# Kernel optimization log

Hardware: AMD Instinct MI355X
Metric: run time of the kernel (lower is better)

Reference implementation:

```python
import jax, jax.numpy as jnp
import numpy as np

N = 50000      # nodes
E = 800000     # edges (before self-loops)
G = 64         # graphs
F_IN = 128     # n_attr
OUT = 128      # size_vect
NEG_SLOPE = 0.2


def setup_inputs() -> dict:
    key = jax.random.key(0)
    ks = jax.random.split(key, 48)
    def rn(i, shape, s=0.05):
        return (jax.random.normal(ks[i], shape, jnp.float32) * s)
    x = jax.random.normal(ks[0], (N, F_IN), jnp.float32)
    src = jax.random.randint(ks[1], (E,), 0, N, jnp.int32)
    dst = jax.random.randint(ks[2], (E,), 0, N, jnp.int32)
    dst = jnp.where(dst == src, (dst + 1) % N, dst)  # no pre-existing self-loops
    edge_index = jnp.stack([src, dst])
    batch = jnp.sort(jax.random.randint(ks[3], (N,), 0, G, jnp.int32))
    inp = {"x": x, "edge_index": edge_index, "batch": batch}
    # GATConv params (heads=1): W [in,out], att_src/att_dst [out], bias [out]
    dims = [(F_IN, 64), (64, 128), (128, 256)]
    for li, (di, do) in enumerate(dims, start=1):
        b = 4 + (li - 1) * 4
        inp[f"W{li}"] = rn(b, (di, do))
        inp[f"asrc{li}"] = rn(b + 1, (do,))
        inp[f"adst{li}"] = rn(b + 2, (do,))
        inp[f"b{li}"] = rn(b + 3, (do,))
    # dense tail: Linear stored as [in,out]
    dense = {"d1": (512, 256), "d2": (256, 128), "d3": (128, 64),
             "mean": (256, 64), "d4": (64, 64), "d5": (64, 128),
             "d6": (128, 256), "d7": (256, OUT)}
    i = 20
    for name, (di, do) in dense.items():
        inp[f"{name}_w"] = rn(i, (di, do))
        inp[f"{name}_b"] = rn(i + 1, (do,))
        i += 2
    return inp


def _gat_conv(x, src, dst, W, a_src, a_dst, b):
    h = x @ W                                   # [N, out]
    e = (h @ a_src)[src] + (h @ a_dst)[dst]     # [E']
    e = jnp.where(e > 0, e, NEG_SLOPE * e)      # LeakyReLU(0.2)
    m = jax.ops.segment_max(e, dst, num_segments=N)
    ex = jnp.exp(e - m[dst])
    denom = jax.ops.segment_sum(ex, dst, num_segments=N)
    alpha = ex / denom[dst]                     # segment softmax over incoming edges
    out = jax.ops.segment_sum(h[src] * alpha[:, None], dst, num_segments=N)
    return out + b


def reference(x, edge_index, batch,
              W1, asrc1, adst1, b1, W2, asrc2, adst2, b2, W3, asrc3, adst3, b3,
              d1_w, d1_b, d2_w, d2_b, d3_w, d3_b, mean_w, mean_b,
              d4_w, d4_b, d5_w, d5_b, d6_w, d6_b, d7_w, d7_b):
    ar = jnp.arange(N, dtype=edge_index.dtype)
    src = jnp.concatenate([edge_index[0], ar])  # add self-loops (PyG default)
    dst = jnp.concatenate([edge_index[1], ar])
    h = _gat_conv(x, src, dst, W1, asrc1, adst1, b1)
    h = _gat_conv(h, src, dst, W2, asrc2, adst2, b2)
    h = _gat_conv(h, src, dst, W3, asrc3, adst3, b3)   # [N, 256]
    x1 = jax.ops.segment_max(h, batch, num_segments=G)
    x2 = jax.ops.segment_sum(h, batch, num_segments=G)
    cnt = jax.ops.segment_sum(jnp.ones((N,), h.dtype), batch, num_segments=G)
    x3 = x2 / jnp.maximum(cnt, 1.0)[:, None]
    z = jnp.concatenate([x1, x2], axis=-1)              # [G, 512]
    z = jax.nn.relu(z @ d1_w + d1_b)
    z = jax.nn.relu(z @ d2_w + d2_b)
    z = jax.nn.relu(z @ d3_w + d3_b)
    z = z * jax.nn.sigmoid(x3 @ mean_w + mean_b)
    z = jax.nn.relu(z @ d4_w + d4_b)                    # dropout = identity (eval)
    z = jax.nn.relu(z @ d5_w + d5_b)
    z = jax.nn.relu(z @ d6_w + d6_b)
    return z @ d7_w + d7_b
```

## Files before the change

kernel.cpp:

```cpp
#include <hip/hip_runtime.h>
#include <hip/hip_bf16.h>
#include <math.h>

#define NN 50000
#define NE 800000
#define NG 64
#define CAP 64

#define NBKT 49
#define BMAX 20480
#define EPB  3125
#define KE   13

typedef unsigned short u16;
typedef __attribute__((ext_vector_type(8))) short short8;
typedef __attribute__((ext_vector_type(4))) float f32x4;

__device__ __forceinline__ float bfu2f(u16 u) {
    return __uint_as_float((unsigned)u << 16);
}
__device__ __forceinline__ u16 f2bfu(float f) {
    __hip_bfloat16 h = __float2bfloat16(f);
    union { __hip_bfloat16 h; u16 u; } c; c.h = h; return c.u;
}

__device__ __forceinline__ unsigned fkey(float f) {
    unsigned u = __float_as_uint(f);
    return (u & 0x80000000u) ? ~u : (u | 0x80000000u);
}
__device__ __forceinline__ float fkey_inv(unsigned k) {
    return (k & 0x80000000u) ? __uint_as_float(k ^ 0x80000000u) : __uint_as_float(~k);
}

__global__ void k_init(int* __restrict__ deg, u16* __restrict__ srcsort, int IB,
                       const float* __restrict__ W0, const float* __restrict__ as0, const float* __restrict__ ad0,
                       u16* __restrict__ Wb0, float* __restrict__ wa0, float* __restrict__ wb0,
                       const float* __restrict__ W1, const float* __restrict__ as1, const float* __restrict__ ad1,
                       u16* __restrict__ Wb1, float* __restrict__ wa1, float* __restrict__ wb1,
                       const float* __restrict__ W2, const float* __restrict__ as2, const float* __restrict__ ad2,
                       const float* __restrict__ b2f, const float* __restrict__ b3f,
                       u16* __restrict__ Wcb, float* __restrict__ bcv,
                       float* __restrict__ wa2c, float* __restrict__ wb2c,
                       float* __restrict__ cst,
                       const int* __restrict__ src, const int* __restrict__ dst,
                       unsigned* __restrict__ ebuf, int* __restrict__ bcur) {
    __shared__ float pas[4], pbs[4];
    __shared__ int hist[NBKT], gbase[NBKT];
    int tid = threadIdx.x;
    if (blockIdx.x < IB) {
        int i = blockIdx.x * 256 + tid;
        if (i < NN) {
            deg[i] = 1;
            srcsort[i << 6] = (u16)i;
        }
        return;
    }
    int b = blockIdx.x - IB;
    if (b < 192) {
        const float *W, *asv, *adv; u16* Wb; float *wa, *wb; int k, dout;
        if (b < 128) { W = W0; asv = as0; adv = ad0; Wb = Wb0; wa = wa0; wb = wb0; k = b;       dout = 64;  }
        else         { W = W1; asv = as1; adv = ad1; Wb = Wb1; wa = wa1; wb = wb1; k = b - 128; dout = 128; }
        float pa = 0.f, pb = 0.f;
        for (int n = tid; n < dout; n += 256) {
            float w = W[(size_t)k * dout + n];
            Wb[(size_t)k * dout + n] = f2bfu(w);
            pa += w * asv[n];
            pb += w * adv[n];
        }
#pragma unroll
        for (int off = 32; off; off >>= 1) {
            pa += __shfl_xor(pa, off);
            pb += __shfl_xor(pb, off);
        }
        if ((tid & 63) == 0) { pas[tid >> 6] = pa; pbs[tid >> 6] = pb; }
        __syncthreads();
        if (tid == 0) {
            wa[k] = pas[0] + pas[1] + pas[2] + pas[3];
            wb[k] = pbs[0] + pbs[1] + pbs[2] + pbs[3];
        }
        return;
    }
    if (b < 256) {
        int k = b - 192;
        int o = tid;
        float wc = 0.f;
        const float* wrow = W1 + (size_t)k * 128;
#pragma unroll 4
        for (int j = 0; j < 128; j++) wc += wrow[j] * W2[(size_t)j * 256 + o];
        Wcb[(size_t)k * 256 + o] = f2bfu(wc);
        float pa = wc * as2[o];
        float pb = wc * ad2[o];
#pragma unroll
        for (int off = 32; off; off >>= 1) {
            pa += __shfl_xor(pa, off);
            pb += __shfl_xor(pb, off);
        }
        if ((tid & 63) == 0) { pas[tid >> 6] = pa; pbs[tid >> 6] = pb; }
        __syncthreads();
        if (tid == 0) {
            wa2c[k] = pas[0] + pas[1] + pas[2] + pas[3];
            wb2c[k] = pbs[0] + pbs[1] + pbs[2] + pbs[3];
        }
        return;
    }
    if (b == 256) {
        int o = tid;
        float t = 0.f;
#pragma unroll 4
        for (int j = 0; j < 128; j++) t += b2f[j] * W2[(size_t)j * 256 + o];
        bcv[o] = t + b3f[o];
        float ps = t * as2[o];
        float pt = t * ad2[o];
#pragma unroll
        for (int off = 32; off; off >>= 1) {
            ps += __shfl_xor(ps, off);
            pt += __shfl_xor(pt, off);
        }
        if ((tid & 63) == 0) { pas[tid >> 6] = ps; pbs[tid >> 6] = pt; }
        __syncthreads();
        if (tid == 0) {
            cst[0] = pas[0] + pas[1] + pas[2] + pas[3];
            cst[1] = pbs[0] + pbs[1] + pbs[2] + pbs[3];
        }
        return;
    }
    {
        int e0 = (b - 257) * EPB;
        if (tid < NBKT) hist[tid] = 0;
        __syncthreads();
        unsigned pk[KE];
        unsigned br[KE];
#pragma unroll
        for (int k = 0; k < KE; k++) {
            int e = tid + k * 256;
            pk[k] = 0; br[k] = 0xffffffffu;
            if (e < EPB) {
                int sv = src[e0 + e];
                int dv = dst[e0 + e];
                int bkt = dv >> 10;
                int r = atomicAdd(&hist[bkt], 1);
                pk[k] = (unsigned)sv | ((unsigned)(dv & 1023) << 16);
                br[k] = ((unsigned)bkt << 16) | (unsigned)r;
            }
        }
        __syncthreads();
        if (tid < NBKT) gbase[tid] = atomicAdd(&bcur[tid], hist[tid]);
        __syncthreads();
#pragma unroll
        for (int k = 0; k < KE; k++) {
            if (br[k] != 0xffffffffu) {
                int bkt = (int)(br[k] >> 16);
                int r   = (int)(br[k] & 0xffffu);
                ebuf[(size_t)bkt * BMAX + gbase[bkt] + r] = pk[k];
            }
        }
    }
}

template<int DIN, int DOUT, bool XF32, bool STIN>
__device__ __forceinline__ void gemm_body(int bx, const void* __restrict__ Xin,
                                          const u16* __restrict__ Wb,
                                          u16* __restrict__ Hb,
                                          const float* __restrict__ bias,
                                          const float* __restrict__ wav,
                                          const float* __restrict__ wbv,
                                          float* __restrict__ sout,
                                          float* __restrict__ tout) {
    constexpr int KS = DIN / 32;
    constexpr int CT = DOUT / 16;
    constexpr int TPW = CT / 4;
    constexpr int STRIDE = DIN + 16;
    __shared__ u16 Xs[64 * STRIDE];
    int tid = threadIdx.x, wave = tid >> 6, lane = tid & 63;
    int quad = lane >> 4, l15 = lane & 15;
    int n0 = bx * 64;

    short8 bfr[TPW][KS];
#pragma unroll
    for (int ct = 0; ct < TPW; ct++) {
        int nb = (wave * TPW + ct) * 16 + l15;
#pragma unroll
        for (int ks = 0; ks < KS; ks++) {
            int kb = ks * 32 + quad * 8;
            short8 b;
#pragma unroll
            for (int j = 0; j < 8; j++) b[j] = (short)Wb[(size_t)(kb + j) * DOUT + nb];
            bfr[ct][ks] = b;
        }
    }

    for (int c = tid; c < 64 * DIN / 8; c += 256) {
        int row = (c * 8) / DIN, col = (c * 8) % DIN;
        int rg = n0 + row; if (rg >= NN) rg = NN - 1;
        u16 v[8];
        if constexpr (XF32) {
            const float* p = (const float*)Xin + (size_t)rg * DIN + col;
            float4 f0 = *(const float4*)p;
            float4 f1 = *(const float4*)(p + 4);
            v[0] = f2bfu(f0.x); v[1] = f2bfu(f0.y); v[2] = f2bfu(f0.z); v[3] = f2bfu(f0.w);
            v[4] = f2bfu(f1.x); v[5] = f2bfu(f1.y); v[6] = f2bfu(f1.z); v[7] = f2bfu(f1.w);
            if constexpr (STIN) {
                float pa = f0.x * wav[col]     + f0.y * wav[col + 1]
                         + f0.z * wav[col + 2] + f0.w * wav[col + 3]
                         + f1.x * wav[col + 4] + f1.y * wav[col + 5]
                         + f1.z * wav[col + 6] + f1.w * wav[col + 7];
                float pb = f0.x * wbv[col]     + f0.y * wbv[col + 1]
                         + f0.z * wbv[col + 2] + f0.w * wbv[col + 3]
                         + f1.x * wbv[col + 4] + f1.y * wbv[col + 5]
                         + f1.z * wbv[col + 6] + f1.w * wbv[col + 7];
                constexpr int RT = DIN / 8;
#pragma unroll
                for (int off = RT / 2; off; off >>= 1) {
                    pa += __shfl_xor(pa, off);
                    pb += __shfl_xor(pb, off);
                }
                if ((tid & (RT - 1)) == 0 && (n0 + row) < NN) {
                    sout[n0 + row] = pa;
                    tout[n0 + row] = pb;
                }
            }
        } else {
            const u16* p = (const u16*)Xin + (size_t)rg * DIN + col;
            ushort4 a = *(const ushort4*)p;
            ushort4 b = *(const ushort4*)(p + 4);
            v[0] = a.x; v[1] = a.y; v[2] = a.z; v[3] = a.w;
            v[4] = b.x; v[5] = b.y; v[6] = b.z; v[7] = b.w;
        }
        u16* d = &Xs[row * STRIDE + col];
#pragma unroll
        for (int j = 0; j < 8; j++) d[j] = v[j];
    }
    __syncthreads();

#pragma unroll
    for (int rt = 0; rt < 4; rt++) {
        short8 afr[KS];
#pragma unroll
        for (int ks = 0; ks < KS; ks++)
            afr[ks] = *(const short8*)&Xs[(rt * 16 + l15) * STRIDE + ks * 32 + quad * 8];
#pragma unroll
        for (int ct = 0; ct < TPW; ct++) {
            f32x4 cf = {0.f, 0.f, 0.f, 0.f};
#pragma unroll
            for (int ks = 0; ks < KS; ks++)
                cf = __builtin_amdgcn_mfma_f32_16x16x32_bf16(afr[ks], bfr[ct][ks], cf, 0, 0, 0);
            int col = (wave * TPW + ct) * 16 + l15;
            float bv = bias ? bias[col] : 0.f;
            int rbase = n0 + rt * 16 + quad * 4;
#pragma unroll
            for (int reg = 0; reg < 4; reg++) {
                int r = rbase + reg;
                if (r < NN) Hb[(size_t)r * DOUT + col] = f2bfu(cf[reg] + bv);
            }
        }
    }
}

__global__ __launch_bounds__(256) void k_front(const unsigned* __restrict__ ebuf,
                                               const int* __restrict__ bcur,
                                               int* __restrict__ deg, u16* __restrict__ srcsort,
                                               const float* __restrict__ x_in,
                                               const u16* __restrict__ Wb0, u16* __restrict__ Hb,
                                               const float* __restrict__ wa, const float* __restrict__ wb,
                                               float* __restrict__ s, float* __restrict__ t) {
    int tid = threadIdx.x;
    if (blockIdx.x < NBKT) {
        __shared__ int cnt[1024];
        int bkt = blockIdx.x;
        int base = bkt << 10;
        for (int i = tid; i < 1024; i += 256) cnt[i] = 1;
        __syncthreads();
        int n = bcur[bkt];
        const unsigned* eb = ebuf + (size_t)bkt * BMAX;
        for (int e = tid; e < n; e += 256) {
            unsigned p = eb[e];
            int sv = (int)(p & 0xffffu);
            int dl = (int)(p >> 16);
            int pos = atomicAdd(&cnt[dl], 1);
            if (pos < CAP) srcsort[((base + dl) << 6) + pos] = (u16)sv;
        }
        __syncthreads();
        for (int i = tid; i < 1024; i += 256) {
            int node = base + i;
            if (node < NN) deg[node] = cnt[i];
        }
        return;
    }
    gemm_body<128, 64, true, true>(blockIdx.x - NBKT, x_in, Wb0, Hb, nullptr, wa, wb, s, t);
}

template<bool BIAS>
__global__ void k_agg1(const int* __restrict__ deg, const u16* __restrict__ srcsort,
                       const float* __restrict__ s, const float* __restrict__ t,
                       const u16* __restrict__ Hb, const float* __restrict__ bias,
                       u16* __restrict__ OUT, const float* __restrict__ wan,
                       const float* __restrict__ wbn, const float* __restrict__ cst,
                       float* __restrict__ sout, float* __restrict__ tout) {
    constexpr int GS = 8;
    constexpr int P  = 8;
    int node = blockIdx.x * 4 + (threadIdx.x >> 6);
    int lane = threadIdx.x & 63;
    if (node >= NN) return;
    int cnt = min(deg[node], CAP);
    float tn = t[node];
    int sv = 0; float ex = 0.f;
    if (lane < cnt) {
        sv = srcsort[(node << 6) + lane];
        float e = s[sv] + tn;
        e = (e > 0.f) ? e : 0.2f * e;
        ex = expf(e);
    }
    float dsum = ex;
#pragma unroll
    for (int off = 32; off; off >>= 1) dsum += __shfl_xor(dsum, off);
    ex *= 1.f / dsum;

    int sg = lane / GS;
    int pg = lane % GS;
    float acc[8];
#pragma unroll
    for (int e = 0; e < 8; e++) acc[e] = 0.f;

    for (int q = 0; q < cnt; q += P) {
        int myq = q + sg;
        int mq = (myq < cnt) ? myq : q;
        float a = __shfl(ex, mq);
        int  idx = __shfl(sv, mq);
        if (myq >= cnt) a = 0.f;
        uint4 u = *(const uint4*)(Hb + (size_t)idx * 64 + pg * 8);
        acc[0] += a * bfu2f((u16)(u.x & 0xffff));
        acc[1] += a * bfu2f((u16)(u.x >> 16));
        acc[2] += a * bfu2f((u16)(u.y & 0xffff));
        acc[3] += a * bfu2f((u16)(u.y >> 16));
        acc[4] += a * bfu2f((u16)(u.z & 0xffff));
        acc[5] += a * bfu2f((u16)(u.z >> 16));
        acc[6] += a * bfu2f((u16)(u.w & 0xffff));
        acc[7] += a * bfu2f((u16)(u.w >> 16));
    }

#pragma unroll
    for (int step = GS; step < 64; step <<= 1) {
#pragma unroll
        for (int e = 0; e < 8; e++) acc[e] += __shfl_xor(acc[e], step);
    }
    if constexpr (BIAS) {
#pragma unroll
        for (int e = 0; e < 8; e++) acc[e] += bias[pg * 8 + e];
    }

    {
        float pa = 0.f, pb = 0.f;
#pragma unroll
        for (int e = 0; e < 8; e++) {
            pa += acc[e] * wan[pg * 8 + e];
            pb += acc[e] * wbn[pg * 8 + e];
        }
#pragma unroll
        for (int off = 32; off; off >>= 1) {
            pa += __shfl_xor(pa, off);
            pb += __shfl_xor(pb, off);
        }
        if (lane == 0) {
            float cs = 0.f, ct_ = 0.f;
            if constexpr (!BIAS) { cs = cst[0]; ct_ = cst[1]; }
            sout[node] = pa * (1.f / P) + cs;
            tout[node] = pb * (1.f / P) + ct_;
        }
    }

    if (sg == 0) {
        uint4 o;
        o.x = (unsigned)f2bfu(acc[0]) | ((unsigned)f2bfu(acc[1]) << 16);
        o.y = (unsigned)f2bfu(acc[2]) | ((unsigned)f2bfu(acc[3]) << 16);
        o.z = (unsigned)f2bfu(acc[4]) | ((unsigned)f2bfu(acc[5]) << 16);
        o.w = (unsigned)f2bfu(acc[6]) | ((unsigned)f2bfu(acc[7]) << 16);
        *(uint4*)(OUT + (size_t)node * 64 + pg * 8) = o;
    }
}

__global__ __launch_bounds__(256) void k_aggemm_pool(const int* __restrict__ deg,
                                                     const u16* __restrict__ srcsort,
                                                     const float* __restrict__ s,
                                                     const float* __restrict__ t,
                                                     const u16* __restrict__ A2,
                                                     const u16* __restrict__ Wb,
                                                     const float* __restrict__ bias,
                                                     const int* __restrict__ batch,
                                                     unsigned* __restrict__ x1k,
                                                     float* __restrict__ x2,
                                                     float* __restrict__ cntg) {
    constexpr int DIN = 64, DOUT = 256;
    constexpr int KS = DIN / 32;
    constexpr int TPW = DOUT / 16 / 4;
    constexpr int STRIDE = DIN + 16;
    __shared__ u16 Xs[64 * STRIDE];
    __shared__ int gID[64];
    int tid = threadIdx.x, wave = tid >> 6, lane = tid & 63;
    int quad = lane >> 4, l15 = lane & 15;
    int n0 = blockIdx.x * 64;

    short8 bfr[TPW][KS];
#pragma unroll
    for (int ct = 0; ct < TPW; ct++) {
        int nb = (wave * TPW + ct) * 16 + l15;
#pragma unroll
        for (int ks = 0; ks < KS; ks++) {
            int kb = ks * 32 + quad * 8;
            short8 b;
#pragma unroll
            for (int j = 0; j < 8; j++) b[j] = (short)Wb[(size_t)(kb + j) * DOUT + nb];
            bfr[ct][ks] = b;
        }
    }

    if (tid < 64) {
        int rg = n0 + tid;
        gID[tid] = batch[(rg < NN) ? rg : (NN - 1)];
    }

    for (int i = 0; i < 16; i++) {
        int row = wave * 16 + i;
        int node = n0 + row;
        if (node < NN) {
            int cnt = min(deg[node], CAP);
            float tn = t[node];
            int sv = 0; float ex = 0.f;
            if (lane < cnt) {
                sv = srcsort[(node << 6) + lane];
                float e = s[sv] + tn;
                e = (e > 0.f) ? e : 0.2f * e;
                ex = expf(e);
            }
            float dsum = ex;
#pragma unroll
            for (int off = 32; off; off >>= 1) dsum += __shfl_xor(dsum, off);
            ex *= 1.f / dsum;

            int sg = lane / 8;
            int pg = lane % 8;
            float acc[8];
#pragma unroll
            for (int e = 0; e < 8; e++) acc[e] = 0.f;
            for (int q = 0; q < cnt; q += 8) {
                int myq = q + sg;
                int mq = (myq < cnt) ? myq : q;
                float a = __shfl(ex, mq);
                int  idx = __shfl(sv, mq);
                if (myq >= cnt) a = 0.f;
                uint4 u = *(const uint4*)(A2 + (size_t)idx * 64 + pg * 8);
                acc[0] += a * bfu2f((u16)(u.x & 0xffff));
                acc[1] += a * bfu2f((u16)(u.x >> 16));
                acc[2] += a * bfu2f((u16)(u.y & 0xffff));
                acc[3] += a * bfu2f((u16)(u.y >> 16));
                acc[4] += a * bfu2f((u16)(u.z & 0xffff));
                acc[5] += a * bfu2f((u16)(u.z >> 16));
                acc[6] += a * bfu2f((u16)(u.w & 0xffff));
                acc[7] += a * bfu2f((u16)(u.w >> 16));
            }
#pragma unroll
            for (int step = 8; step < 64; step <<= 1) {
#pragma unroll
                for (int e = 0; e < 8; e++) acc[e] += __shfl_xor(acc[e], step);
            }
            if (sg == 0) {
                u16* d = &Xs[row * STRIDE + pg * 8];
#pragma unroll
                for (int e = 0; e < 8; e++) d[e] = f2bfu(acc[e]);
            }
        } else {
            if (lane < 8) {
                u16* d = &Xs[row * STRIDE + lane * 8];
#pragma unroll
                for (int e = 0; e < 8; e++) d[e] = 0;
            }
        }
    }
    __syncthreads();

    f32x4 acc2[4][TPW];
#pragma unroll
    for (int rt = 0; rt < 4; rt++) {
        short8 afr[KS];
#pragma unroll
        for (int ks = 0; ks < KS; ks++)
            afr[ks] = *(const short8*)&Xs[(rt * 16 + l15) * STRIDE + ks * 32 + quad * 8];
#pragma unroll
        for (int ct = 0; ct < TPW; ct++) {
            f32x4 cf = {0.f, 0.f, 0.f, 0.f};
#pragma unroll
            for (int ks = 0; ks < KS; ks++)
                cf = __builtin_amdgcn_mfma_f32_16x16x32_bf16(afr[ks], bfr[ct][ks], cf, 0, 0, 0);
            acc2[rt][ct] = cf;
        }
    }

    float bv[TPW];
#pragma unroll
    for (int ct = 0; ct < TPW; ct++) bv[ct] = bias[(wave * TPW + ct) * 16 + l15];
    int gmin = gID[0];
    int lastv = (n0 + 63 < NN) ? 63 : (NN - 1 - n0);
    int gmax = gID[lastv];
    for (int g = gmin; g <= gmax; g++) {
        float m[TPW], ss[TPW];
#pragma unroll
        for (int ct = 0; ct < TPW; ct++) { m[ct] = -INFINITY; ss[ct] = 0.f; }
#pragma unroll
        for (int rt = 0; rt < 4; rt++) {
#pragma unroll
            for (int reg = 0; reg < 4; reg++) {
                int lr = rt * 16 + quad * 4 + reg;
                bool ok = (n0 + lr < NN) && (gID[lr] == g);
#pragma unroll
                for (int ct = 0; ct < TPW; ct++) {
                    float v = acc2[rt][ct][reg] + bv[ct];
                    if (ok) { m[ct] = fmaxf(m[ct], v); ss[ct] += v; }
                }
            }
        }
#pragma unroll
        for (int ct = 0; ct < TPW; ct++) {
            m[ct]  = fmaxf(m[ct],  __shfl_xor(m[ct], 16));
            ss[ct] += __shfl_xor(ss[ct], 16);
            m[ct]  = fmaxf(m[ct],  __shfl_xor(m[ct], 32));
            ss[ct] += __shfl_xor(ss[ct], 32);
        }
        if (lane < 16) {
#pragma unroll
            for (int ct = 0; ct < TPW; ct++) {
                int col = (wave * TPW + ct) * 16 + l15;
                if (m[ct] > -INFINITY) {
                    atomicMax(&x1k[(size_t)g * 256 + col], fkey(m[ct]));
                    atomicAdd(&x2[(size_t)g * 256 + col], ss[ct]);
                }
            }
        }
    }
    if (tid == 0) {
        int cg = gID[0], cc = 0;
        for (int i = 0; i < 64; i++) {
            if (n0 + i >= NN) break;
            if (gID[i] != cg) { atomicAdd(&cntg[cg], (float)cc); cg = gID[i]; cc = 0; }
            cc++;
        }
        if (cc > 0) atomicAdd(&cntg[cg], (float)cc);
    }
}

template<int DIN, int DOUT, int ACT>
__device__ __forceinline__ void dense_layer(const float* __restrict__ in,
                                            const float* __restrict__ W,
                                            const float* __restrict__ B,
                                            float* __restrict__ out, int o,
                                            float* __restrict__ red) {
    constexpr int T = 1024 / DOUT;
    constexpr int KS = DIN / T;
    int oo = o % DOUT;
    int kk = o / DOUT;
    int kbase = kk * KS;
    float p0 = 0.f, p1 = 0.f, p2 = 0.f, p3 = 0.f;
#pragma unroll 4
    for (int k = 0; k < KS; k += 4) {
        p0 += in[kbase + k]     * W[(size_t)(kbase + k) * DOUT + oo];
        p1 += in[kbase + k + 1] * W[(size_t)(kbase + k + 1) * DOUT + oo];
        p2 += in[kbase + k + 2] * W[(size_t)(kbase + k + 2) * DOUT + oo];
        p3 += in[kbase + k + 3] * W[(size_t)(kbase + k + 3) * DOUT + oo];
    }
    float p = (p0 + p1) + (p2 + p3);
    red[o] = p;
    __syncthreads();
    if (o < DOUT) {
#pragma unroll
        for (int tt = 1; tt < T; tt++) p += red[oo + tt * DOUT];
        p += B[oo];
        if constexpr (ACT == 1) p = fmaxf(p, 0.f);
        else if constexpr (ACT == 2) p = 1.f / (1.f + expf(-p));
        out[oo] = p;
    }
    __syncthreads();
}

__global__ __launch_bounds__(1024) void k_tail(const unsigned* __restrict__ x1k, const float* __restrict__ x2,
                       const float* __restrict__ cnt,
                       const float* __restrict__ d1w, const float* __restrict__ d1b,
                       const float* __restrict__ d2w, const float* __restrict__ d2b,
                       const float* __restrict__ d3w, const float* __restrict__ d3b,
                       const float* __restrict__ mw,  const float* __restrict__ mb,
                       const float* __restrict__ d4w, const float* __restrict__ d4b,
                       const float* __restrict__ d5w, const float* __restrict__ d5b,
                       const float* __restrict__ d6w, const float* __restrict__ d6b,
                       const float* __restrict__ d7w, const float* __restrict__ d7b,
                       float* __restrict__ out) {
    __shared__ float z[512];
    __shared__ float A[256];
    __shared__ float Bf[256];
    __shared__ float red[1024];
    __shared__ float x3s[256];
    __shared__ float gbuf[64];
    int g = blockIdx.x, o = threadIdx.x;
    if (o < 256) {
        float c = fmaxf(cnt[g], 1.f);
        float sv = x2[(size_t)g * 256 + o];
        z[o] = fkey_inv(x1k[(size_t)g * 256 + o]);
        z[256 + o] = sv;
        x3s[o] = sv / c;
    }
    __syncthreads();
    dense_layer<512, 256, 1>(z,   d1w, d1b, A,    o, red);
    dense_layer<256, 128, 1>(A,   d2w, d2b, Bf,   o, red);
    dense_layer<128,  64, 1>(Bf,  d3w, d3b, A,    o, red);
    dense_layer<256,  64, 2>(x3s, mw,  mb,  gbuf, o, red);
    if (o < 64) A[o] *= gbuf[o];
    __syncthreads();
    dense_layer< 64,  64, 1>(A,   d4w, d4b, Bf,   o, red);
    dense_layer< 64, 128, 1>(Bf,  d5w, d5b, A,    o, red);
    dense_layer<128, 256, 1>(A,   d6w, d6b, z,    o, red);
    dense_layer<256, 128, 0>(z,   d7w, d7b, A,    o, red);
    if (o < 128) out[(size_t)g * 128 + o] = A[o];
}

extern "C" void kernel_launch(void* const* d_in, const int* in_sizes, int n_in,
                              void* d_out, int out_size, void* d_ws, size_t ws_size,
                              hipStream_t stream) {
    const float* x_in  = (const float*)d_in[0];
    const int*   ei    = (const int*)d_in[1];
    const int*   batch = (const int*)d_in[2];
    const int* src = ei;
    const int* dst = ei + NE;

    const float* Wl[3]  = { (const float*)d_in[3], (const float*)d_in[7],  (const float*)d_in[11] };
    const float* asl[3] = { (const float*)d_in[4], (const float*)d_in[8],  (const float*)d_in[12] };
    const float* adl[3] = { (const float*)d_in[5], (const float*)d_in[9],  (const float*)d_in[13] };
    const float* bl[3]  = { (const float*)d_in[6], (const float*)d_in[10], (const float*)d_in[14] };

    const float* d1w = (const float*)d_in[15]; const float* d1b = (const float*)d_in[16];
    const float* d2w = (const float*)d_in[17]; const float* d2b = (const float*)d_in[18];
    const float* d3w = (const float*)d_in[19]; const float* d3b = (const float*)d_in[20];
    const float* mw  = (const float*)d_in[21]; const float* mb  = (const float*)d_in[22];
    const float* d4w = (const float*)d_in[23]; const float* d4b = (const float*)d_in[24];
    const float* d5w = (const float*)d_in[25]; const float* d5b = (const float*)d_in[26];
    const float* d6w = (const float*)d_in[27]; const float* d6b = (const float*)d_in[28];
    const float* d7w = (const float*)d_in[29]; const float* d7b = (const float*)d_in[30];

    float* ws = (float*)d_ws;
    size_t off = 0;
    u16* Hb1 = (u16*)(ws + off); off += (size_t)NN * 32;
    u16* Xb1 = (u16*)(ws + off); off += (size_t)NN * 32;
    u16* A2  = (u16*)(ws + off); off += (size_t)NN * 32;
    float* bcv = ws + off; off += 256;
    float* cst = ws + off; off += 64;
    unsigned* ebuf = (unsigned*)(ws + off); off += (size_t)NBKT * BMAX;
    float* sA = ws + off; off += NN;
    float* tA = ws + off; off += NN;
    float* sB = ws + off; off += NN;
    float* tB = ws + off; off += NN;
    u16* Wb0 = (u16*)(ws + off); off += (128 * 64) / 2;
    u16* Wb1 = (u16*)(ws + off); off += (64 * 128) / 2;
    u16* Wcb = (u16*)(ws + off); off += (64 * 256) / 2;
    float* wa0 = ws + off; off += 128;  float* wb0 = ws + off; off += 128;
    float* wa1 = ws + off; off += 64;   float* wb1 = ws + off; off += 64;
    float* wa2c = ws + off; off += 64;  float* wb2c = ws + off; off += 64;
    unsigned* x1k = (unsigned*)(ws + off); off += NG * 256;
    float* x2    = ws + off; off += NG * 256;
    float* cnt   = ws + off; off += NG;
    int* bcur    = (int*)(ws + off); off += 64;
    int* ip      = (int*)(ws + off);
    int* deg     = ip;               ip += NN;
    u16* srcsort = (u16*)ip;         ip += (NN * CAP) / 2;

    const int GB = (NN + 63) / 64;
    const int AB = (NN + 3) / 4;
    const int IB = (NN + 255) / 256;

    hipMemsetAsync(x1k, 0, (size_t)(NG * 512 + NG + 64) * 4, stream);
    k_init<<<IB + 513, 256, 0, stream>>>(deg, srcsort, IB,
                                         Wl[0], asl[0], adl[0], Wb0, wa0, wb0,
                                         Wl[1], asl[1], adl[1], Wb1, wa1, wb1,
                                         Wl[2], asl[2], adl[2], bl[1], bl[2],
                                         Wcb, bcv, wa2c, wb2c, cst,
                                         src, dst, ebuf, bcur);
    k_front<<<NBKT + GB, 256, 0, stream>>>(ebuf, bcur, deg, srcsort,
                                           x_in, Wb0, Hb1, wa0, wb0, sA, tA);

    k_agg1<true><<<AB, 256, 0, stream>>>(deg, srcsort, sA, tA, Hb1, bl[0],
                                         Xb1, wa1, wb1, nullptr, sB, tB);

    k_agg1<false><<<AB, 256, 0, stream>>>(deg, srcsort, sB, tB, Xb1, nullptr,
                                          A2, wa2c, wb2c, cst, sA, tA);

    k_aggemm_pool<<<GB, 256, 0, stream>>>(deg, srcsort, sA, tA, A2, Wcb, bcv,
                                          batch, x1k, x2, cnt);

    k_tail<<<NG, 1024, 0, stream>>>(x1k, x2, cnt,
                                    d1w, d1b, d2w, d2b, d3w, d3b, mw, mb,
                                    d4w, d4b, d5w, d5b, d6w, d6b, d7w, d7b,
                                    (float*)d_out);
}
```

Before: 344.3 us.

## Split fused layer-3 aggregation+GEMM+pool into separate gather and GEMM kernels

The fused kernel did the attention-weighted neighbor gather for 64 nodes serially per wave (16 nodes per wave) before the MFMA GEMM and pooling. This splits it into a dedicated aggregation kernel with one wave per node, which writes a bf16 intermediate buffer, and a GEMM+pool kernel that loads that buffer into shared memory. The aim is more parallelism and latency hiding for the irregular gather, at the cost of an extra global round trip for a 50000x64 bf16 buffer and one more kernel launch.

```diff
diff --git a/kernel.cpp b/kernel.cpp
--- a/kernel.cpp
+++ b/kernel.cpp
@@ -378,17 +378,74 @@
     }
 }
 
-__global__ __launch_bounds__(256) void k_aggemm_pool(const int* __restrict__ deg,
-                                                     const u16* __restrict__ srcsort,
-                                                     const float* __restrict__ s,
-                                                     const float* __restrict__ t,
-                                                     const u16* __restrict__ A2,
-                                                     const u16* __restrict__ Wb,
-                                                     const float* __restrict__ bias,
-                                                     const int* __restrict__ batch,
-                                                     unsigned* __restrict__ x1k,
-                                                     float* __restrict__ x2,
-                                                     float* __restrict__ cntg) {
+__global__ void k_aggX64(const int* __restrict__ deg, const u16* __restrict__ srcsort,
+                         const float* __restrict__ s, const float* __restrict__ t,
+                         const u16* __restrict__ X, u16* __restrict__ OUT) {
+    constexpr int GS = 8;
+    constexpr int P  = 8;
+    int node = blockIdx.x * 4 + (threadIdx.x >> 6);
+    int lane = threadIdx.x & 63;
+    if (node >= NN) return;
+    int cnt = min(deg[node], CAP);
+    float tn = t[node];
+    int sv = 0; float ex = 0.f;
+    if (lane < cnt) {
+        sv = srcsort[(node << 6) + lane];
+        float e = s[sv] + tn;
+        e = (e > 0.f) ? e : 0.2f * e;
+        ex = expf(e);
+    }
+    float dsum = ex;
+#pragma unroll
+    for (int off = 32; off; off >>= 1) dsum += __shfl_xor(dsum, off);
+    ex *= 1.f / dsum;
+
+    int sg = lane / GS;
+    int pg = lane % GS;
+    float acc[8];
+#pragma unroll
+    for (int e = 0; e < 8; e++) acc[e] = 0.f;
+
+    for (int q = 0; q < cnt; q += P) {
+        int myq = q + sg;
+        int mq = (myq < cnt) ? myq : q;
+        float a = __shfl(ex, mq);
+        int  idx = __shfl(sv, mq);
+        if (myq >= cnt) a = 0.f;
+        uint4 u = *(const uint4*)(X + (size_t)idx * 64 + pg * 8);
+        acc[0] += a * bfu2f((u16)(u.x & 0xffff));
+        acc[1] += a * bfu2f((u16)(u.x >> 16));
+        acc[2] += a * bfu2f((u16)(u.y & 0xffff));
+        acc[3] += a * bfu2f((u16)(u.y >> 16));
+        acc[4] += a * bfu2f((u16)(u.z & 0xffff));
+        acc[5] += a * bfu2f((u16)(u.z >> 16));
+        acc[6] += a * bfu2f((u16)(u.w & 0xffff));
+        acc[7] += a * bfu2f((u16)(u.w >> 16));
+    }
+
+#pragma unroll
+    for (int step = GS; step < 64; step <<= 1) {
+#pragma unroll
+        for (int e = 0; e < 8; e++) acc[e] += __shfl_xor(acc[e], step);
+    }
+
+    if (sg == 0) {
+        uint4 o;
+        o.x = (unsigned)f2bfu(acc[0]) | ((unsigned)f2bfu(acc[1]) << 16);
+        o.y = (unsigned)f2bfu(acc[2]) | ((unsigned)f2bfu(acc[3]) << 16);
+        o.z = (unsigned)f2bfu(acc[4]) | ((unsigned)f2bfu(acc[5]) << 16);
+        o.w = (unsigned)f2bfu(acc[6]) | ((unsigned)f2bfu(acc[7]) << 16);
+        *(uint4*)(OUT + (size_t)node * 64 + pg * 8) = o;
+    }
+}
+
+__global__ __launch_bounds__(256) void k_gemm_pool(const u16* __restrict__ Xin,
+                                                   const u16* __restrict__ Wb,
+                                                   const float* __restrict__ bias,
+                                                   const int* __restrict__ batch,
+                                                   unsigned* __restrict__ x1k,
+                                                   float* __restrict__ x2,
+                                                   float* __restrict__ cntg) {
     constexpr int DIN = 64, DOUT = 256;
     constexpr int KS = DIN / 32;
     constexpr int TPW = DOUT / 16 / 4;
@@ -418,62 +475,15 @@
         gID[tid] = batch[(rg < NN) ? rg : (NN - 1)];
     }
 
-    for (int i = 0; i < 16; i++) {
-        int row = wave * 16 + i;
-        int node = n0 + row;
-        if (node < NN) {
-            int cnt = min(deg[node], CAP);
-            float tn = t[node];
-            int sv = 0; float ex = 0.f;
-            if (lane < cnt) {
-                sv = srcsort[(node << 6) + lane];
-                float e = s[sv] + tn;
-                e = (e > 0.f) ? e : 0.2f * e;
-                ex = expf(e);
-            }
-            float dsum = ex;
-#pragma unroll
-            for (int off = 32; off; off >>= 1) dsum += __shfl_xor(dsum, off);
-            ex *= 1.f / dsum;
-
-            int sg = lane / 8;
-            int pg = lane % 8;
-            float acc[8];
-#pragma unroll
-            for (int e = 0; e < 8; e++) acc[e] = 0.f;
-            for (int q = 0; q < cnt; q += 8) {
-                int myq = q + sg;
-                int mq = (myq < cnt) ? myq : q;
-                float a = __shfl(ex, mq);
-                int  idx = __shfl(sv, mq);
-                if (myq >= cnt) a = 0.f;
-                uint4 u = *(const uint4*)(A2 + (size_t)idx * 64 + pg * 8);
-                acc[0] += a * bfu2f((u16)(u.x & 0xffff));
-                acc[1] += a * bfu2f((u16)(u.x >> 16));
-                acc[2] += a * bfu2f((u16)(u.y & 0xffff));
-                acc[3] += a * bfu2f((u16)(u.y >> 16));
-                acc[4] += a * bfu2f((u16)(u.z & 0xffff));
-                acc[5] += a * bfu2f((u16)(u.z >> 16));
-                acc[6] += a * bfu2f((u16)(u.w & 0xffff));
-                acc[7] += a * bfu2f((u16)(u.w >> 16));
-            }
-#pragma unroll
-            for (int step = 8; step < 64; step <<= 1) {
-#pragma unroll
-                for (int e = 0; e < 8; e++) acc[e] += __shfl_xor(acc[e], step);
-            }
-            if (sg == 0) {
-                u16* d = &Xs[row * STRIDE + pg * 8];
-#pragma unroll
-                for (int e = 0; e < 8; e++) d[e] = f2bfu(acc[e]);
-            }
-        } else {
-            if (lane < 8) {
-                u16* d = &Xs[row * STRIDE + lane * 8];
-#pragma unroll
-                for (int e = 0; e < 8; e++) d[e] = 0;
-            }
-        }
+    for (int c = tid; c < 64 * DIN / 8; c += 256) {
+        int row = (c * 8) / DIN, col = (c * 8) % DIN;
+        int rg = n0 + row; if (rg >= NN) rg = NN - 1;
+        const u16* p = Xin + (size_t)rg * DIN + col;
+        ushort4 a = *(const ushort4*)p;
+        ushort4 b = *(const ushort4*)(p + 4);
+        u16* d = &Xs[row * STRIDE + col];
+        d[0] = a.x; d[1] = a.y; d[2] = a.z; d[3] = a.w;
+        d[4] = b.x; d[5] = b.y; d[6] = b.z; d[7] = b.w;
     }
     __syncthreads();
 
@@ -646,6 +656,7 @@
     u16* Hb1 = (u16*)(ws + off); off += (size_t)NN * 32;
     u16* Xb1 = (u16*)(ws + off); off += (size_t)NN * 32;
     u16* A2  = (u16*)(ws + off); off += (size_t)NN * 32;
+    u16* B3  = (u16*)(ws + off); off += (size_t)NN * 32;
     float* bcv = ws + off; off += 256;
     float* cst = ws + off; off += 64;
     unsigned* ebuf = (unsigned*)(ws + off); off += (size_t)NBKT * BMAX;
@@ -687,8 +698,8 @@
     k_agg1<false><<<AB, 256, 0, stream>>>(deg, srcsort, sB, tB, Xb1, nullptr,
                                           A2, wa2c, wb2c, cst, sA, tA);
 
-    k_aggemm_pool<<<GB, 256, 0, stream>>>(deg, srcsort, sA, tA, A2, Wcb, bcv,
-                                          batch, x1k, x2, cnt);
+    k_aggX64<<<AB, 256, 0, stream>>>(deg, srcsort, sA, tA, A2, B3);
+    k_gemm_pool<<<GB, 256, 0, stream>>>(B3, Wcb, bcv, batch, x1k, x2, cnt);
 
     k_tail<<<NG, 1024, 0, stream>>>(x1k, x2, cnt,
                                     d1w, d1b, d2w, d2b, d3w, d3b, mw, mb,
```

Measured after the change: 293.7 us. 14.7% less time.
